# Kernel optimization log

Measured on AMD Instinct MI355X. Metric: run time of the kernel, lower is better.

## Reference

```python
import jax, jax.numpy as jnp
import numpy as np

N = 100000
E = 1600000
NFEAT = 128
NHID1 = 128
NHID2 = 128
NCLASS = 40


def setup_inputs() -> dict:
    key = jax.random.key(0)
    ks = jax.random.split(key, 16)
    x = jax.random.normal(ks[0], (N, NFEAT), dtype=jnp.float32)
    src = jax.random.randint(ks[1], (E,), 0, N, dtype=jnp.int32)
    dst = jax.random.randint(ks[2], (E,), 0, N, dtype=jnp.int32)
    s = 0.05
    params = {
        # SAGE layer 1: self branch and neighbor branch
        'w1s': jax.random.normal(ks[3], (NFEAT, NHID1), dtype=jnp.float32) * s,
        'b1s': jnp.zeros((NHID1,), dtype=jnp.float32),
        'w1n': jax.random.normal(ks[4], (NFEAT, NHID1), dtype=jnp.float32) * s,
        'b1n': jnp.zeros((NHID1,), dtype=jnp.float32),
        # SAGE layer 2 (input dim 2*NHID1)
        'w2s': jax.random.normal(ks[5], (2 * NHID1, NHID2), dtype=jnp.float32) * s,
        'b2s': jnp.zeros((NHID2,), dtype=jnp.float32),
        'w2n': jax.random.normal(ks[6], (2 * NHID1, NHID2), dtype=jnp.float32) * s,
        'b2n': jnp.zeros((NHID2,), dtype=jnp.float32),
        # final linear head (input dim 2*NHID2)
        'wfc': jax.random.normal(ks[7], (2 * NHID2, NCLASS), dtype=jnp.float32) * s,
        'bfc': jnp.zeros((NCLASS,), dtype=jnp.float32),
    }
    return {'x': x, 'src': src, 'dst': dst, **params}


def _neigh_mean(h, src, dst, n_nodes):
    # mean aggregation == spmm(row-normalized adj, h), via segment sum over edges
    msg = jax.ops.segment_sum(h[src], dst, num_segments=n_nodes)  # [N, d]
    cnt = jax.ops.segment_sum(jnp.ones((src.shape[0],), h.dtype), dst, num_segments=n_nodes)
    return msg / jnp.maximum(cnt, 1.0)[:, None]


def _sage_layer(h, src, dst, ws, bs, wn, bn):
    neigh = _neigh_mean(h, src, dst, h.shape[0])
    return jnp.concatenate([h @ ws + bs, neigh @ wn + bn], axis=1)


def _l2_normalize(h, eps=1e-12):
    nrm = jnp.sqrt(jnp.sum(h * h, axis=1, keepdims=True))
    return h / jnp.maximum(nrm, eps)


def reference(x, src, dst, w1s, b1s, w1n, b1n, w2s, b2s, w2n, b2n, wfc, bfc):
    h = jax.nn.relu(_sage_layer(x, src, dst, w1s, b1s, w1n, b1n))  # [N, 2*NHID1]
    h = _l2_normalize(h)
    # dropout is identity in eval mode
    h = jax.nn.relu(_sage_layer(h, src, dst, w2s, b2s, w2n, b2n))  # [N, 2*NHID2]
    h = _l2_normalize(h)
    return h @ wfc + bfc  # [N, NCLASS]
```

## Files before the change

### kernel.cpp

```cpp
#include <hip/hip_runtime.h>
#include <hip/hip_bf16.h>


#define N_NODES 100000
#define N_EDGES 1600000
#define NBUCK   196
#define BCAP    12288
#define CHUNK   4096

typedef unsigned short u16;
typedef unsigned int u32;
typedef __bf16 bf16x8 __attribute__((ext_vector_type(8)));
typedef float  f32x4  __attribute__((ext_vector_type(4)));

__device__ __forceinline__ u16 f2b(float f) {
  unsigned x = __builtin_bit_cast(unsigned, f);
  unsigned r = x + 0x7fffu + ((x >> 16) & 1u);
  return (u16)(r >> 16);
}
__device__ __forceinline__ float b2f(u16 u) {
  return __builtin_bit_cast(float, (unsigned)u << 16);
}
__device__ __forceinline__ bf16x8 ldfrag(const u16* p) {
  uint4 u = *reinterpret_cast<const uint4*>(p);
  return __builtin_bit_cast(bf16x8, u);
}
__device__ __forceinline__ void unpack8(uint4 u, float* f) {
  f[0] = __builtin_bit_cast(float, u.x << 16);
  f[1] = __builtin_bit_cast(float, u.x & 0xffff0000u);
  f[2] = __builtin_bit_cast(float, u.y << 16);
  f[3] = __builtin_bit_cast(float, u.y & 0xffff0000u);
  f[4] = __builtin_bit_cast(float, u.z << 16);
  f[5] = __builtin_bit_cast(float, u.z & 0xffff0000u);
  f[6] = __builtin_bit_cast(float, u.w << 16);
  f[7] = __builtin_bit_cast(float, u.w & 0xffff0000u);
}
__device__ __forceinline__ uint4 pack8(const float* f) {
  uint4 u;
  u.x = (u32)f2b(f[0]) | ((u32)f2b(f[1]) << 16);
  u.y = (u32)f2b(f[2]) | ((u32)f2b(f[3]) << 16);
  u.z = (u32)f2b(f[4]) | ((u32)f2b(f[5]) << 16);
  u.w = (u32)f2b(f[6]) | ((u32)f2b(f[7]) << 16);
  return u;
}

__global__ __launch_bounds__(256) void prep_weights(
    const float* __restrict__ w1s, const float* __restrict__ w1n,
    const float* __restrict__ w2s, const float* __restrict__ w2n,
    const float* __restrict__ wfc,
    u16* __restrict__ WT1, u16* __restrict__ WT2, u16* __restrict__ WFCT) {
  int i = blockIdx.x * 256 + threadIdx.x;
  if (i < 32768) {
    int c = i >> 7, k = i & 127;
    float v = (c < 128) ? w1s[k * 128 + c] : w1n[k * 128 + (c - 128)];
    WT1[c * 128 + k] = f2b(v);
  } else if (i < 32768 + 65536) {
    int j = i - 32768;
    int c = j >> 8, k = j & 255;
    float v = (c < 128) ? w2s[k * 128 + c] : w2n[k * 128 + (c - 128)];
    WT2[c * 256 + k] = f2b(v);
  } else {
    int j = i - 98304;
    int c = j >> 8, k = j & 255;
    float v = (c < 40) ? wfc[k * 40 + c] : 0.f;
    WFCT[c * 256 + k] = f2b(v);
  }
}

__device__ __forceinline__ int wave_incl_scan(int x, int lane) {
#pragma unroll
  for (int d = 1; d < 64; d <<= 1) {
    int n = __shfl_up(x, d, 64);
    if (lane >= d) x += n;
  }
  return x;
}

__global__ __launch_bounds__(256) void bucket_kernel(
    const int* __restrict__ src, const int* __restrict__ dst,
    int* __restrict__ cntg, u32* __restrict__ pairBuf) {
  __shared__ unsigned hist[NBUCK];
  __shared__ unsigned gbase[NBUCK];
  __shared__ int sws[4];
  __shared__ u32 stage[CHUNK];
  __shared__ int tgt[CHUNK];
  const int tid = threadIdx.x, lane = tid & 63, wid = tid >> 6;
  const int e0 = blockIdx.x * CHUNK;

  for (int i = tid; i < NBUCK; i += 256) hist[i] = 0u;
  __syncthreads();

  u32 myW[16];
  int myR[16], myB[16];
#pragma unroll
  for (int k = 0; k < 16; ++k) {
    int e = e0 + k * 256 + tid;
    if (e < N_EDGES) {
      unsigned d = (unsigned)dst[e];
      myW[k] = ((d & 511u) << 17) | (unsigned)src[e];
      myB[k] = (int)(d >> 9);
      myR[k] = (int)atomicAdd(&hist[myB[k]], 1u);
    } else {
      myB[k] = -1;
    }
  }
  __syncthreads();

  int cnt = (tid < NBUCK) ? (int)hist[tid] : 0;
  int inc = wave_incl_scan(cnt, lane);
  if (lane == 63) sws[wid] = inc;
  __syncthreads();
  if (wid == 0) {
    int s = (lane < 4) ? sws[lane] : 0;
    s = wave_incl_scan(s, lane);
    if (lane < 4) sws[lane] = s;
  }
  __syncthreads();
  int excl = (wid ? sws[wid - 1] : 0) + inc - cnt;
  int gofs = 0;
  if (tid < NBUCK && cnt > 0) gofs = tid * BCAP + atomicAdd(&cntg[tid], cnt);
  __syncthreads();
  if (tid < NBUCK) {
    hist[tid] = (unsigned)excl;
    gbase[tid] = (unsigned)gofs;
  }
  __syncthreads();

#pragma unroll
  for (int k = 0; k < 16; ++k) {
    if (myB[k] >= 0) {
      int slot = (int)hist[myB[k]] + myR[k];
      stage[slot] = myW[k];
      tgt[slot] = (int)gbase[myB[k]] + myR[k];
    }
  }
  __syncthreads();
  int nvalid = N_EDGES - e0;
  if (nvalid > CHUNK) nvalid = CHUNK;
  for (int i = tid; i < nvalid; i += 256) pairBuf[tgt[i]] = stage[i];
}

__global__ __launch_bounds__(512) void csr_build(
    const u32* __restrict__ pairBuf, const int* __restrict__ cntg,
    int* __restrict__ rowptr, int* __restrict__ csr) {
  __shared__ int lcnt[512];
  __shared__ int lofs[512];
  __shared__ int sws[8];
  __shared__ int s_eb;
  __shared__ int cstage[10240];
  const int b = blockIdx.x, tid = threadIdx.x;
  const int lane = tid & 63, wid = tid >> 6;

  {
    int v = (tid < b) ? cntg[tid] : 0;
#pragma unroll
    for (int off = 1; off < 64; off <<= 1) v += __shfl_xor(v, off, 64);
    if (lane == 0) sws[wid] = v;
    __syncthreads();
    if (tid == 0) {
      int t = 0;
#pragma unroll
      for (int i = 0; i < 8; ++i) t += sws[i];
      s_eb = t;
    }
    __syncthreads();
  }
  const int eb = s_eb;
  int nb = cntg[b];
  if (nb > BCAP) nb = BCAP;
  if (nb > 10240) nb = 10240;
  const u32* pp = pairBuf + (size_t)b * BCAP;
  __syncthreads();

  lcnt[tid] = 0;
  __syncthreads();
  for (int i = tid; i < nb; i += 512) atomicAdd(&lcnt[(pp[i] >> 17) & 511], 1);
  __syncthreads();
  int v = lcnt[tid];
  int inc = wave_incl_scan(v, lane);
  if (lane == 63) sws[wid] = inc;
  __syncthreads();
  if (wid == 0) {
    int s = (lane < 8) ? sws[lane] : 0;
    s = wave_incl_scan(s, lane);
    if (lane < 8) sws[lane] = s;
  }
  __syncthreads();
  int excl = (wid ? sws[wid - 1] : 0) + inc - v;
  int node = b * 512 + tid;
  if (node <= N_NODES) rowptr[node] = eb + excl;
  lofs[tid] = excl;
  __syncthreads();
  for (int i = tid; i < nb; i += 512) {
    u32 pr = pp[i];
    int pos = atomicAdd(&lofs[(pr >> 17) & 511], 1);
    cstage[pos] = (int)(pr & 0x1FFFFu);
  }
  __syncthreads();
  for (int i = tid; i < nb; i += 512) csr[eb + i] = cstage[i];
}

template <int K, bool AF32>
__global__ __launch_bounds__(256) void gemm_kernel(
    const void* __restrict__ Av, const u16* __restrict__ WT,
    u16* __restrict__ Cs, u16* __restrict__ Cn) {
  constexpr int RB = K * 2;
  constexpr int LOG2RB = (K == 128) ? 8 : 9;
  constexpr int KS = K / 32;
  __shared__ u16 lb[128 * K];

  const int tid = threadIdx.x;
  const int half = blockIdx.x & 1;
  u16* __restrict__ Cout = half ? Cn : Cs;

  const u16* Wsrc = WT + (size_t)half * 128 * K;
  char* lbc = reinterpret_cast<char*>(lb);
#pragma unroll
  for (int i = tid; i < 128 * K / 8; i += 256) {
    uint4 v = *reinterpret_cast<const uint4*>(Wsrc + i * 8);
    int byte = i * 16;
    int swz = byte ^ (((byte >> LOG2RB) & 7) << 4);
    *reinterpret_cast<uint4*>(lbc + swz) = v;
  }
  __syncthreads();

  const int w = tid >> 6, lane = tid & 63;
  const int lrow = lane & 15, lk = lane >> 4;
  const int xr = (lrow & 7) << 4;
  const int stride = gridDim.x >> 1;

  for (int chunk = blockIdx.x >> 1; chunk * 128 < N_NODES; chunk += stride) {
    const int rbase = chunk * 128 + w * 32;
    bf16x8 af[2][KS];
#pragma unroll
    for (int rt = 0; rt < 2; ++rt) {
      int r = rbase + rt * 16 + lrow;
      if (r >= N_NODES) r = N_NODES - 1;
      if constexpr (AF32) {
        const float* ap = (const float*)Av + (size_t)r * K + lk * 8;
#pragma unroll
        for (int ks = 0; ks < KS; ++ks) {
          float4 f0 = *reinterpret_cast<const float4*>(ap + ks * 32);
          float4 f1 = *reinterpret_cast<const float4*>(ap + ks * 32 + 4);
          float f[8] = {f0.x, f0.y, f0.z, f0.w, f1.x, f1.y, f1.z, f1.w};
          af[rt][ks] = __builtin_bit_cast(bf16x8, pack8(f));
        }
      } else {
        const u16* ap = (const u16*)Av + (size_t)r * K + lk * 8;
#pragma unroll
        for (int ks = 0; ks < KS; ++ks) af[rt][ks] = ldfrag(ap + ks * 32);
      }
    }
    f32x4 acc[2][8];
#pragma unroll
    for (int rt = 0; rt < 2; ++rt)
#pragma unroll
      for (int ct = 0; ct < 8; ++ct) acc[rt][ct] = f32x4{0.f, 0.f, 0.f, 0.f};

#pragma unroll
    for (int ks = 0; ks < KS; ++ks) {
#pragma unroll
      for (int ct = 0; ct < 8; ++ct) {
        int byte = (ct * 16 + lrow) * RB + ks * 64 + lk * 16;
        bf16x8 b = __builtin_bit_cast(
            bf16x8, *reinterpret_cast<const uint4*>(lbc + (byte ^ xr)));
        acc[0][ct] = __builtin_amdgcn_mfma_f32_16x16x32_bf16(af[0][ks], b, acc[0][ct], 0, 0, 0);
        acc[1][ct] = __builtin_amdgcn_mfma_f32_16x16x32_bf16(af[1][ks], b, acc[1][ct], 0, 0, 0);
      }
    }
#pragma unroll
    for (int rt = 0; rt < 2; ++rt) {
#pragma unroll
      for (int j = 0; j < 4; ++j) {
        int r = rbase + rt * 16 + lk * 4 + j;
        if (r < N_NODES) {
          u16* cp = Cout + (size_t)r * 128 + lrow;
#pragma unroll
          for (int ct = 0; ct < 8; ++ct) cp[ct * 16] = f2b(acc[rt][ct][j]);
        }
      }
    }
  }
}

__global__ __launch_bounds__(256) void agg_epi_kernel(
    const u16* __restrict__ Xs, const u16* __restrict__ Xn,
    const int* __restrict__ rowptr, const int* __restrict__ csr,
    const float* __restrict__ bs, const float* __restrict__ bn,
    u16* __restrict__ H) {
  int node = (int)((blockIdx.x * 256 + threadIdx.x) >> 6);
  int lane = threadIdx.x & 63;
  if (node >= N_NODES) return;
  const int g = lane >> 4;
  const int lc = lane & 15;
  int beg = rowptr[node], end = rowptr[node + 1];

  float acc[8] = {0.f, 0.f, 0.f, 0.f, 0.f, 0.f, 0.f, 0.f};
  const u16* colbase = Xn + lc * 8;
  for (int j = beg; j < end; j += 4) {
    int e = j + g;
    int s = (e < end) ? csr[e] : 0;
    uint4 u = *reinterpret_cast<const uint4*>(colbase + (size_t)s * 128);
    if (e < end) {
      float f[8];
      unpack8(u, f);
#pragma unroll
      for (int i = 0; i < 8; ++i) acc[i] += f[i];
    }
  }
#pragma unroll
  for (int i = 0; i < 8; ++i) {
    acc[i] += __shfl_xor(acc[i], 32, 64);
    acc[i] += __shfl_xor(acc[i], 16, 64);
  }
  int d = end - beg;
  float inv = 1.f / (float)(d > 0 ? d : 1);

  uint4 sv4 = *reinterpret_cast<const uint4*>(Xs + (size_t)node * 128 + lc * 8);
  float sf[8];
  unpack8(sv4, sf);
  float4 b0 = *reinterpret_cast<const float4*>(bs + lc * 8);
  float4 b1 = *reinterpret_cast<const float4*>(bs + lc * 8 + 4);
  float4 c0 = *reinterpret_cast<const float4*>(bn + lc * 8);
  float4 c1 = *reinterpret_cast<const float4*>(bn + lc * 8 + 4);
  float bsv[8] = {b0.x, b0.y, b0.z, b0.w, b1.x, b1.y, b1.z, b1.w};
  float bnv[8] = {c0.x, c0.y, c0.z, c0.w, c1.x, c1.y, c1.z, c1.w};
  float nf[8];
  float ss = 0.f;
#pragma unroll
  for (int i = 0; i < 8; ++i) {
    sf[i] = fmaxf(sf[i] + bsv[i], 0.f);
    nf[i] = fmaxf(acc[i] * inv + bnv[i], 0.f);
    ss += sf[i] * sf[i] + nf[i] * nf[i];
  }
  ss += __shfl_xor(ss, 1, 64);
  ss += __shfl_xor(ss, 2, 64);
  ss += __shfl_xor(ss, 4, 64);
  ss += __shfl_xor(ss, 8, 64);
  float sc = 1.f / fmaxf(sqrtf(ss), 1e-12f);
#pragma unroll
  for (int i = 0; i < 8; ++i) {
    sf[i] *= sc;
    nf[i] *= sc;
  }
  if (g == 0) {
    *reinterpret_cast<uint4*>(H + (size_t)node * 256 + lc * 8) = pack8(sf);
  } else if (g == 1) {
    *reinterpret_cast<uint4*>(H + (size_t)node * 256 + 128 + lc * 8) = pack8(nf);
  }
}

__global__ __launch_bounds__(256) void fc_kernel(const u16* __restrict__ H2,
                                                 const u16* __restrict__ WFCT,
                                                 const float* __restrict__ bfc,
                                                 float* __restrict__ Out) {
  __shared__ u16 lb[48 * 256];
  char* lbc = reinterpret_cast<char*>(lb);
  const int tid = threadIdx.x;
#pragma unroll
  for (int i = tid; i < 48 * 256 / 8; i += 256) {
    uint4 v = *reinterpret_cast<const uint4*>(WFCT + i * 8);
    int byte = i * 16;
    int swz = byte ^ (((byte >> 9) & 7) << 4);
    *reinterpret_cast<uint4*>(lbc + swz) = v;
  }
  __syncthreads();
  const int w = tid >> 6, lane = tid & 63;
  const int lrow = lane & 15, lk = lane >> 4;
  const int xr = (lrow & 7) << 4;
  const int rbase = blockIdx.x * 64 + w * 16;

  bf16x8 af[8];
  {
    int r = rbase + lrow;
    if (r >= N_NODES) r = N_NODES - 1;
    const u16* ap = H2 + (size_t)r * 256 + lk * 8;
#pragma unroll
    for (int ks = 0; ks < 8; ++ks) af[ks] = ldfrag(ap + ks * 32);
  }
  f32x4 acc[3];
#pragma unroll
  for (int ct = 0; ct < 3; ++ct) acc[ct] = f32x4{0.f, 0.f, 0.f, 0.f};
#pragma unroll
  for (int ks = 0; ks < 8; ++ks) {
#pragma unroll
    for (int ct = 0; ct < 3; ++ct) {
      int byte = (ct * 16 + lrow) * 512 + ks * 64 + lk * 16;
      bf16x8 b = __builtin_bit_cast(
          bf16x8, *reinterpret_cast<const uint4*>(lbc + (byte ^ xr)));
      acc[ct] = __builtin_amdgcn_mfma_f32_16x16x32_bf16(af[ks], b, acc[ct], 0, 0, 0);
    }
  }
#pragma unroll
  for (int j = 0; j < 4; ++j) {
    int r = rbase + lk * 4 + j;
    if (r < N_NODES) {
#pragma unroll
      for (int ct = 0; ct < 3; ++ct) {
        int col = ct * 16 + lrow;
        if (col < 40) Out[(size_t)r * 40 + col] = acc[ct][j] + bfc[col];
      }
    }
  }
}

extern "C" void kernel_launch(void* const* d_in, const int* in_sizes, int n_in,
                              void* d_out, int out_size, void* d_ws, size_t ws_size,
                              hipStream_t stream) {
  const float* x = (const float*)d_in[0];
  const int* src = (const int*)d_in[1];
  const int* dst = (const int*)d_in[2];
  const float* w1s = (const float*)d_in[3];
  const float* b1s = (const float*)d_in[4];
  const float* w1n = (const float*)d_in[5];
  const float* b1n = (const float*)d_in[6];
  const float* w2s = (const float*)d_in[7];
  const float* b2s = (const float*)d_in[8];
  const float* w2n = (const float*)d_in[9];
  const float* b2n = (const float*)d_in[10];
  const float* wfc = (const float*)d_in[11];
  const float* bfc = (const float*)d_in[12];
  float* out = (float*)d_out;

  char* p = (char*)d_ws;
  auto alloc = [&](size_t bytes) {
    char* r = p;
    p += (bytes + 255) & ~(size_t)255;
    return r;
  };
  u16* XWs = (u16*)alloc((size_t)N_NODES * 128 * 2);
  u16* XWn = (u16*)alloc((size_t)N_NODES * 128 * 2);
  u16* h1 = (u16*)alloc((size_t)N_NODES * 256 * 2);
  u16* WT1 = (u16*)alloc(32768 * 2);
  u16* WT2 = (u16*)alloc(65536 * 2);
  u16* WFCT = (u16*)alloc(12288 * 2);
  u32* pairBuf = (u32*)alloc((size_t)NBUCK * BCAP * 4);
  int* cntg = (int*)alloc(NBUCK * 4);
  int* rowptr = (int*)alloc((N_NODES + 1) * 4);
  int* csr = (int*)alloc((size_t)N_EDGES * 4);
  u16* h2 = h1;

  hipMemsetAsync(cntg, 0, NBUCK * 4, stream);
  prep_weights<<<432, 256, 0, stream>>>(w1s, w1n, w2s, w2n, wfc, WT1, WT2, WFCT);
  bucket_kernel<<<391, 256, 0, stream>>>(src, dst, cntg, pairBuf);
  csr_build<<<NBUCK, 512, 0, stream>>>(pairBuf, cntg, rowptr, csr);

  gemm_kernel<128, true><<<1024, 256, 0, stream>>>(x, WT1, XWs, XWn);
  agg_epi_kernel<<<25000, 256, 0, stream>>>(XWs, XWn, rowptr, csr, b1s, b1n, h1);
  gemm_kernel<256, false><<<512, 256, 0, stream>>>(h1, WT2, XWs, XWn);
  agg_epi_kernel<<<25000, 256, 0, stream>>>(XWs, XWn, rowptr, csr, b2s, b2n, h2);
  fc_kernel<<<1563, 256, 0, stream>>>(h2, WFCT, bfc, out);
}
```

Before: 386.1 us.

## Pad CSR rows to multiples of eight, fuse layer-2 aggregation with FC head

Builds a per-bucket padded CSR. Each node's neighbor list is rounded up to a multiple of eight and filled with a dummy node whose XWn row is zeroed, so the aggregation loop runs branch-free and issues two gathers per iteration. The global prefix sum in csr_build and the separate memset are removed. The GEMMs become dedicated 512-thread kernels that compute both halves per block, and the final aggregation is fused with the FC matmul through shared memory so h2 is never written out. The cost is extra padded edge reads and larger CSR storage.

Result: faster. 359.9 us (-6.8%).

```diff
diff --git a/kernel.cpp b/kernel.cpp
--- a/kernel.cpp
+++ b/kernel.cpp
@@ -6,6 +6,7 @@
 #define N_EDGES 1600000
 #define NBUCK   196
 #define BCAP    12288
+#define PB_CAP  14336
 #define CHUNK   4096
 
 typedef unsigned short u16;
@@ -17,9 +18,6 @@
   unsigned x = __builtin_bit_cast(unsigned, f);
   unsigned r = x + 0x7fffu + ((x >> 16) & 1u);
   return (u16)(r >> 16);
-}
-__device__ __forceinline__ float b2f(u16 u) {
-  return __builtin_bit_cast(float, (unsigned)u << 16);
 }
 __device__ __forceinline__ bf16x8 ldfrag(const u16* p) {
   uint4 u = *reinterpret_cast<const uint4*>(p);
@@ -48,7 +46,8 @@
     const float* __restrict__ w1s, const float* __restrict__ w1n,
     const float* __restrict__ w2s, const float* __restrict__ w2n,
     const float* __restrict__ wfc,
-    u16* __restrict__ WT1, u16* __restrict__ WT2, u16* __restrict__ WFCT) {
+    u16* __restrict__ WT1, u16* __restrict__ WT2, u16* __restrict__ WFCT,
+    int* __restrict__ cntg, u16* __restrict__ XWn) {
   int i = blockIdx.x * 256 + threadIdx.x;
   if (i < 32768) {
     int c = i >> 7, k = i & 127;
@@ -59,11 +58,15 @@
     int c = j >> 8, k = j & 255;
     float v = (c < 128) ? w2s[k * 128 + c] : w2n[k * 128 + (c - 128)];
     WT2[c * 256 + k] = f2b(v);
-  } else {
+  } else if (i < 98304 + 12288) {
     int j = i - 98304;
     int c = j >> 8, k = j & 255;
     float v = (c < 40) ? wfc[k * 40 + c] : 0.f;
     WFCT[c * 256 + k] = f2b(v);
+  } else {
+    int t = threadIdx.x;
+    if (t < NBUCK) cntg[t] = 0;
+    if (t >= 128 && t < 256) XWn[(size_t)N_NODES * 128 + (t - 128)] = 0;
   }
 }
 
@@ -142,42 +145,24 @@
 
 __global__ __launch_bounds__(512) void csr_build(
     const u32* __restrict__ pairBuf, const int* __restrict__ cntg,
-    int* __restrict__ rowptr, int* __restrict__ csr) {
+    int* __restrict__ rowptr, int* __restrict__ degA, int* __restrict__ csr) {
   __shared__ int lcnt[512];
   __shared__ int lofs[512];
   __shared__ int sws[8];
-  __shared__ int s_eb;
-  __shared__ int cstage[10240];
+  __shared__ int cstage[PB_CAP];
   const int b = blockIdx.x, tid = threadIdx.x;
   const int lane = tid & 63, wid = tid >> 6;
-
-  {
-    int v = (tid < b) ? cntg[tid] : 0;
-#pragma unroll
-    for (int off = 1; off < 64; off <<= 1) v += __shfl_xor(v, off, 64);
-    if (lane == 0) sws[wid] = v;
-    __syncthreads();
-    if (tid == 0) {
-      int t = 0;
-#pragma unroll
-      for (int i = 0; i < 8; ++i) t += sws[i];
-      s_eb = t;
-    }
-    __syncthreads();
-  }
-  const int eb = s_eb;
   int nb = cntg[b];
   if (nb > BCAP) nb = BCAP;
-  if (nb > 10240) nb = 10240;
   const u32* pp = pairBuf + (size_t)b * BCAP;
-  __syncthreads();
 
   lcnt[tid] = 0;
   __syncthreads();
   for (int i = tid; i < nb; i += 512) atomicAdd(&lcnt[(pp[i] >> 17) & 511], 1);
   __syncthreads();
-  int v = lcnt[tid];
-  int inc = wave_incl_scan(v, lane);
+  int dg = lcnt[tid];
+  int pd = (dg + 7) & ~7;
+  int inc = wave_incl_scan(pd, lane);
   if (lane == 63) sws[wid] = inc;
   __syncthreads();
   if (wid == 0) {
@@ -186,138 +171,57 @@
     if (lane < 8) sws[lane] = s;
   }
   __syncthreads();
-  int excl = (wid ? sws[wid - 1] : 0) + inc - v;
+  int excl = (wid ? sws[wid - 1] : 0) + inc - pd;
+  int ptot = sws[7];
   int node = b * 512 + tid;
-  if (node <= N_NODES) rowptr[node] = eb + excl;
+  if (node < N_NODES) {
+    rowptr[node] = b * PB_CAP + excl;
+    degA[node] = dg;
+  }
   lofs[tid] = excl;
   __syncthreads();
   for (int i = tid; i < nb; i += 512) {
     u32 pr = pp[i];
     int pos = atomicAdd(&lofs[(pr >> 17) & 511], 1);
-    cstage[pos] = (int)(pr & 0x1FFFFu);
-  }
-  __syncthreads();
-  for (int i = tid; i < nb; i += 512) csr[eb + i] = cstage[i];
-}
-
-template <int K, bool AF32>
-__global__ __launch_bounds__(256) void gemm_kernel(
-    const void* __restrict__ Av, const u16* __restrict__ WT,
-    u16* __restrict__ Cs, u16* __restrict__ Cn) {
-  constexpr int RB = K * 2;
-  constexpr int LOG2RB = (K == 128) ? 8 : 9;
-  constexpr int KS = K / 32;
-  __shared__ u16 lb[128 * K];
-
-  const int tid = threadIdx.x;
-  const int half = blockIdx.x & 1;
-  u16* __restrict__ Cout = half ? Cn : Cs;
-
-  const u16* Wsrc = WT + (size_t)half * 128 * K;
-  char* lbc = reinterpret_cast<char*>(lb);
-#pragma unroll
-  for (int i = tid; i < 128 * K / 8; i += 256) {
-    uint4 v = *reinterpret_cast<const uint4*>(Wsrc + i * 8);
-    int byte = i * 16;
-    int swz = byte ^ (((byte >> LOG2RB) & 7) << 4);
-    *reinterpret_cast<uint4*>(lbc + swz) = v;
-  }
-  __syncthreads();
-
-  const int w = tid >> 6, lane = tid & 63;
-  const int lrow = lane & 15, lk = lane >> 4;
-  const int xr = (lrow & 7) << 4;
-  const int stride = gridDim.x >> 1;
-
-  for (int chunk = blockIdx.x >> 1; chunk * 128 < N_NODES; chunk += stride) {
-    const int rbase = chunk * 128 + w * 32;
-    bf16x8 af[2][KS];
-#pragma unroll
-    for (int rt = 0; rt < 2; ++rt) {
-      int r = rbase + rt * 16 + lrow;
-      if (r >= N_NODES) r = N_NODES - 1;
-      if constexpr (AF32) {
-        const float* ap = (const float*)Av + (size_t)r * K + lk * 8;
-#pragma unroll
-        for (int ks = 0; ks < KS; ++ks) {
-          float4 f0 = *reinterpret_cast<const float4*>(ap + ks * 32);
-          float4 f1 = *reinterpret_cast<const float4*>(ap + ks * 32 + 4);
-          float f[8] = {f0.x, f0.y, f0.z, f0.w, f1.x, f1.y, f1.z, f1.w};
-          af[rt][ks] = __builtin_bit_cast(bf16x8, pack8(f));
-        }
-      } else {
-        const u16* ap = (const u16*)Av + (size_t)r * K + lk * 8;
-#pragma unroll
-        for (int ks = 0; ks < KS; ++ks) af[rt][ks] = ldfrag(ap + ks * 32);
-      }
-    }
-    f32x4 acc[2][8];
-#pragma unroll
-    for (int rt = 0; rt < 2; ++rt)
-#pragma unroll
-      for (int ct = 0; ct < 8; ++ct) acc[rt][ct] = f32x4{0.f, 0.f, 0.f, 0.f};
-
-#pragma unroll
-    for (int ks = 0; ks < KS; ++ks) {
-#pragma unroll
-      for (int ct = 0; ct < 8; ++ct) {
-        int byte = (ct * 16 + lrow) * RB + ks * 64 + lk * 16;
-        bf16x8 b = __builtin_bit_cast(
-            bf16x8, *reinterpret_cast<const uint4*>(lbc + (byte ^ xr)));
-        acc[0][ct] = __builtin_amdgcn_mfma_f32_16x16x32_bf16(af[0][ks], b, acc[0][ct], 0, 0, 0);
-        acc[1][ct] = __builtin_amdgcn_mfma_f32_16x16x32_bf16(af[1][ks], b, acc[1][ct], 0, 0, 0);
-      }
-    }
-#pragma unroll
-    for (int rt = 0; rt < 2; ++rt) {
-#pragma unroll
-      for (int j = 0; j < 4; ++j) {
-        int r = rbase + rt * 16 + lk * 4 + j;
-        if (r < N_NODES) {
-          u16* cp = Cout + (size_t)r * 128 + lrow;
-#pragma unroll
-          for (int ct = 0; ct < 8; ++ct) cp[ct * 16] = f2b(acc[rt][ct][j]);
-        }
-      }
-    }
-  }
-}
-
-__global__ __launch_bounds__(256) void agg_epi_kernel(
+    if (pos < PB_CAP) cstage[pos] = (int)(pr & 0x1FFFFu);
+  }
+  __syncthreads();
+  for (int k = excl + dg; k < excl + pd; ++k)
+    if (k < PB_CAP) cstage[k] = N_NODES;
+  __syncthreads();
+  if (ptot > PB_CAP) ptot = PB_CAP;
+  for (int i = tid; i < ptot; i += 512) csr[b * PB_CAP + i] = cstage[i];
+}
+
+__device__ __forceinline__ void agg_node(
     const u16* __restrict__ Xs, const u16* __restrict__ Xn,
-    const int* __restrict__ rowptr, const int* __restrict__ csr,
-    const float* __restrict__ bs, const float* __restrict__ bn,
-    u16* __restrict__ H) {
-  int node = (int)((blockIdx.x * 256 + threadIdx.x) >> 6);
-  int lane = threadIdx.x & 63;
-  if (node >= N_NODES) return;
-  const int g = lane >> 4;
-  const int lc = lane & 15;
-  int beg = rowptr[node], end = rowptr[node + 1];
-
+    const int* __restrict__ rowptr, const int* __restrict__ degA,
+    const int* __restrict__ csr, const float* __restrict__ bs,
+    const float* __restrict__ bn, int node, int g, int lc,
+    float* sf, float* nf) {
+  int beg = rowptr[node], dg = degA[node];
+  int cnt = (dg + 7) & ~7;
   float acc[8] = {0.f, 0.f, 0.f, 0.f, 0.f, 0.f, 0.f, 0.f};
   const u16* colbase = Xn + lc * 8;
-  for (int j = beg; j < end; j += 4) {
-    int e = j + g;
-    int s = (e < end) ? csr[e] : 0;
-    uint4 u = *reinterpret_cast<const uint4*>(colbase + (size_t)s * 128);
-    if (e < end) {
-      float f[8];
-      unpack8(u, f);
-#pragma unroll
-      for (int i = 0; i < 8; ++i) acc[i] += f[i];
-    }
+  const int* cp = csr + beg;
+  for (int j = 0; j < cnt; j += 8) {
+    int s0 = cp[j + g];
+    int s1 = cp[j + 4 + g];
+    uint4 u0 = *reinterpret_cast<const uint4*>(colbase + (size_t)s0 * 128);
+    uint4 u1 = *reinterpret_cast<const uint4*>(colbase + (size_t)s1 * 128);
+    float f0[8], f1[8];
+    unpack8(u0, f0);
+    unpack8(u1, f1);
+#pragma unroll
+    for (int i = 0; i < 8; ++i) acc[i] += f0[i] + f1[i];
   }
 #pragma unroll
   for (int i = 0; i < 8; ++i) {
     acc[i] += __shfl_xor(acc[i], 32, 64);
     acc[i] += __shfl_xor(acc[i], 16, 64);
   }
-  int d = end - beg;
-  float inv = 1.f / (float)(d > 0 ? d : 1);
-
+  float inv = 1.f / (float)(dg > 0 ? dg : 1);
   uint4 sv4 = *reinterpret_cast<const uint4*>(Xs + (size_t)node * 128 + lc * 8);
-  float sf[8];
   unpack8(sv4, sf);
   float4 b0 = *reinterpret_cast<const float4*>(bs + lc * 8);
   float4 b1 = *reinterpret_cast<const float4*>(bs + lc * 8 + 4);
@@ -325,7 +229,6 @@
   float4 c1 = *reinterpret_cast<const float4*>(bn + lc * 8 + 4);
   float bsv[8] = {b0.x, b0.y, b0.z, b0.w, b1.x, b1.y, b1.z, b1.w};
   float bnv[8] = {c0.x, c0.y, c0.z, c0.w, c1.x, c1.y, c1.z, c1.w};
-  float nf[8];
   float ss = 0.f;
 #pragma unroll
   for (int i = 0; i < 8; ++i) {
@@ -343,6 +246,19 @@
     sf[i] *= sc;
     nf[i] *= sc;
   }
+}
+
+__global__ __launch_bounds__(256) void agg_epi_kernel(
+    const u16* __restrict__ Xs, const u16* __restrict__ Xn,
+    const int* __restrict__ rowptr, const int* __restrict__ degA,
+    const int* __restrict__ csr, const float* __restrict__ bs,
+    const float* __restrict__ bn, u16* __restrict__ H) {
+  int node = (int)((blockIdx.x * 256 + threadIdx.x) >> 6);
+  int lane = threadIdx.x & 63;
+  if (node >= N_NODES) return;
+  const int g = lane >> 4, lc = lane & 15;
+  float sf[8], nf[8];
+  agg_node(Xs, Xn, rowptr, degA, csr, bs, bn, node, g, lc, sf, nf);
   if (g == 0) {
     *reinterpret_cast<uint4*>(H + (size_t)node * 256 + lc * 8) = pack8(sf);
   } else if (g == 1) {
@@ -350,57 +266,177 @@
   }
 }
 
-__global__ __launch_bounds__(256) void fc_kernel(const u16* __restrict__ H2,
-                                                 const u16* __restrict__ WFCT,
-                                                 const float* __restrict__ bfc,
-                                                 float* __restrict__ Out) {
-  __shared__ u16 lb[48 * 256];
+__global__ __launch_bounds__(512) void agg_fc_kernel(
+    const u16* __restrict__ Xs, const u16* __restrict__ Xn,
+    const int* __restrict__ rowptr, const int* __restrict__ degA,
+    const int* __restrict__ csr, const float* __restrict__ bs,
+    const float* __restrict__ bn, const u16* __restrict__ WFCT,
+    const float* __restrict__ bfc, float* __restrict__ Out) {
+  __shared__ u16 hh[32][264];
+  __shared__ u16 wf[48][264];
+  const int tid = threadIdx.x, w = tid >> 6, lane = tid & 63;
+  const int g = lane >> 4, lc = lane & 15;
+  const int nb0 = blockIdx.x * 32;
+
+  for (int i = tid; i < 1536; i += 512) {
+    int row = i >> 5, col = (i & 31) * 8;
+    *reinterpret_cast<uint4*>(&wf[row][col]) =
+        *reinterpret_cast<const uint4*>(WFCT + row * 256 + col);
+  }
+
+  for (int t = 0; t < 4; ++t) {
+    int r = w * 4 + t;
+    int node = nb0 + r;
+    if (node < N_NODES) {
+      float sf[8], nf[8];
+      agg_node(Xs, Xn, rowptr, degA, csr, bs, bn, node, g, lc, sf, nf);
+      if (g == 0) {
+        *reinterpret_cast<uint4*>(&hh[r][lc * 8]) = pack8(sf);
+      } else if (g == 1) {
+        *reinterpret_cast<uint4*>(&hh[r][128 + lc * 8]) = pack8(nf);
+      }
+    } else {
+      uint4 z = {0u, 0u, 0u, 0u};
+      if (g == 0) *reinterpret_cast<uint4*>(&hh[r][lc * 8]) = z;
+      else if (g == 1) *reinterpret_cast<uint4*>(&hh[r][128 + lc * 8]) = z;
+    }
+  }
+  __syncthreads();
+
+  const int rt = w & 1, cg = w >> 1;
+  if (cg < 3) {
+    const int lrow = lane & 15, lk = lane >> 4;
+    f32x4 acc = {0.f, 0.f, 0.f, 0.f};
+#pragma unroll
+    for (int ks = 0; ks < 8; ++ks) {
+      bf16x8 a = ldfrag(&hh[rt * 16 + lrow][ks * 32 + lk * 8]);
+      bf16x8 b = ldfrag(&wf[cg * 16 + lrow][ks * 32 + lk * 8]);
+      acc = __builtin_amdgcn_mfma_f32_16x16x32_bf16(a, b, acc, 0, 0, 0);
+    }
+#pragma unroll
+    for (int j = 0; j < 4; ++j) {
+      int row = nb0 + rt * 16 + lk * 4 + j;
+      int col = cg * 16 + lrow;
+      if (row < N_NODES && col < 40) Out[(size_t)row * 40 + col] = acc[j] + bfc[col];
+    }
+  }
+}
+
+__global__ __launch_bounds__(512) void gemm1_kernel(
+    const float* __restrict__ A, const u16* __restrict__ WT,
+    u16* __restrict__ Cs, u16* __restrict__ Cn) {
+  __shared__ u16 lb[256 * 128];
   char* lbc = reinterpret_cast<char*>(lb);
   const int tid = threadIdx.x;
-#pragma unroll
-  for (int i = tid; i < 48 * 256 / 8; i += 256) {
-    uint4 v = *reinterpret_cast<const uint4*>(WFCT + i * 8);
+  for (int i = tid; i < 4096; i += 512) {
+    uint4 v = *reinterpret_cast<const uint4*>(WT + i * 8);
     int byte = i * 16;
-    int swz = byte ^ (((byte >> 9) & 7) << 4);
+    int swz = byte ^ (((byte >> 8) & 7) << 4);
     *reinterpret_cast<uint4*>(lbc + swz) = v;
   }
-  __syncthreads();
+
   const int w = tid >> 6, lane = tid & 63;
   const int lrow = lane & 15, lk = lane >> 4;
   const int xr = (lrow & 7) << 4;
-  const int rbase = blockIdx.x * 64 + w * 16;
+  const int rbase = blockIdx.x * 128 + w * 16;
+
+  bf16x8 af[4];
+  {
+    int r = rbase + lrow;
+    if (r >= N_NODES) r = N_NODES - 1;
+    const float* ap = A + (size_t)r * 128 + lk * 8;
+#pragma unroll
+    for (int ks = 0; ks < 4; ++ks) {
+      float4 f0 = *reinterpret_cast<const float4*>(ap + ks * 32);
+      float4 f1 = *reinterpret_cast<const float4*>(ap + ks * 32 + 4);
+      float f[8] = {f0.x, f0.y, f0.z, f0.w, f1.x, f1.y, f1.z, f1.w};
+      af[ks] = __builtin_bit_cast(bf16x8, pack8(f));
+    }
+  }
+  __syncthreads();
+
+  f32x4 acc[16];
+#pragma unroll
+  for (int ct = 0; ct < 16; ++ct) acc[ct] = f32x4{0.f, 0.f, 0.f, 0.f};
+#pragma unroll
+  for (int ks = 0; ks < 4; ++ks) {
+#pragma unroll
+    for (int ct = 0; ct < 16; ++ct) {
+      int byte = (ct * 16 + lrow) * 256 + ks * 64 + lk * 16;
+      bf16x8 b = __builtin_bit_cast(
+          bf16x8, *reinterpret_cast<const uint4*>(lbc + (byte ^ xr)));
+      acc[ct] = __builtin_amdgcn_mfma_f32_16x16x32_bf16(af[ks], b, acc[ct], 0, 0, 0);
+    }
+  }
+#pragma unroll
+  for (int j = 0; j < 4; ++j) {
+    int r = rbase + lk * 4 + j;
+    if (r < N_NODES) {
+      u16* cs = Cs + (size_t)r * 128 + lrow;
+      u16* cn = Cn + (size_t)r * 128 + lrow;
+#pragma unroll
+      for (int ct = 0; ct < 8; ++ct) cs[ct * 16] = f2b(acc[ct][j]);
+#pragma unroll
+      for (int ct = 0; ct < 8; ++ct) cn[ct * 16] = f2b(acc[8 + ct][j]);
+    }
+  }
+}
+
+__global__ __launch_bounds__(512) void gemm2_kernel(
+    const u16* __restrict__ A, const u16* __restrict__ WT,
+    u16* __restrict__ Cs, u16* __restrict__ Cn) {
+  __shared__ u16 lb[128 * 256];
+  char* lbc = reinterpret_cast<char*>(lb);
+  const int tid = threadIdx.x;
+  const int w = tid >> 6, lane = tid & 63;
+  const int lrow = lane & 15, lk = lane >> 4;
+  const int xr = (lrow & 7) << 4;
+  const int rbase = blockIdx.x * 128 + w * 16;
 
   bf16x8 af[8];
   {
     int r = rbase + lrow;
     if (r >= N_NODES) r = N_NODES - 1;
-    const u16* ap = H2 + (size_t)r * 256 + lk * 8;
+    const u16* ap = A + (size_t)r * 256 + lk * 8;
 #pragma unroll
     for (int ks = 0; ks < 8; ++ks) af[ks] = ldfrag(ap + ks * 32);
   }
-  f32x4 acc[3];
-#pragma unroll
-  for (int ct = 0; ct < 3; ++ct) acc[ct] = f32x4{0.f, 0.f, 0.f, 0.f};
-#pragma unroll
-  for (int ks = 0; ks < 8; ++ks) {
-#pragma unroll
-    for (int ct = 0; ct < 3; ++ct) {
-      int byte = (ct * 16 + lrow) * 512 + ks * 64 + lk * 16;
-      bf16x8 b = __builtin_bit_cast(
-          bf16x8, *reinterpret_cast<const uint4*>(lbc + (byte ^ xr)));
-      acc[ct] = __builtin_amdgcn_mfma_f32_16x16x32_bf16(af[ks], b, acc[ct], 0, 0, 0);
-    }
-  }
-#pragma unroll
-  for (int j = 0; j < 4; ++j) {
-    int r = rbase + lk * 4 + j;
-    if (r < N_NODES) {
-#pragma unroll
-      for (int ct = 0; ct < 3; ++ct) {
-        int col = ct * 16 + lrow;
-        if (col < 40) Out[(size_t)r * 40 + col] = acc[ct][j] + bfc[col];
+
+#pragma unroll
+  for (int half = 0; half < 2; ++half) {
+    const u16* Wsrc = WT + (size_t)half * 128 * 256;
+    for (int i = tid; i < 4096; i += 512) {
+      uint4 v = *reinterpret_cast<const uint4*>(Wsrc + i * 8);
+      int byte = i * 16;
+      int swz = byte ^ (((byte >> 9) & 7) << 4);
+      *reinterpret_cast<uint4*>(lbc + swz) = v;
+    }
+    __syncthreads();
+
+    f32x4 acc[8];
+#pragma unroll
+    for (int ct = 0; ct < 8; ++ct) acc[ct] = f32x4{0.f, 0.f, 0.f, 0.f};
+#pragma unroll
+    for (int ks = 0; ks < 8; ++ks) {
+#pragma unroll
+      for (int ct = 0; ct < 8; ++ct) {
+        int byte = (ct * 16 + lrow) * 512 + ks * 64 + lk * 16;
+        bf16x8 b = __builtin_bit_cast(
+            bf16x8, *reinterpret_cast<const uint4*>(lbc + (byte ^ xr)));
+        acc[ct] = __builtin_amdgcn_mfma_f32_16x16x32_bf16(af[ks], b, acc[ct], 0, 0, 0);
       }
     }
+    u16* __restrict__ Cout = half ? Cn : Cs;
+#pragma unroll
+    for (int j = 0; j < 4; ++j) {
+      int r = rbase + lk * 4 + j;
+      if (r < N_NODES) {
+        u16* cp = Cout + (size_t)r * 128 + lrow;
+#pragma unroll
+        for (int ct = 0; ct < 8; ++ct) cp[ct * 16] = f2b(acc[ct][j]);
+      }
+    }
+    __syncthreads();
   }
 }
 
@@ -429,25 +465,25 @@
     return r;
   };
   u16* XWs = (u16*)alloc((size_t)N_NODES * 128 * 2);
-  u16* XWn = (u16*)alloc((size_t)N_NODES * 128 * 2);
+  u16* XWn = (u16*)alloc(((size_t)N_NODES + 1) * 128 * 2);
   u16* h1 = (u16*)alloc((size_t)N_NODES * 256 * 2);
   u16* WT1 = (u16*)alloc(32768 * 2);
   u16* WT2 = (u16*)alloc(65536 * 2);
   u16* WFCT = (u16*)alloc(12288 * 2);
   u32* pairBuf = (u32*)alloc((size_t)NBUCK * BCAP * 4);
   int* cntg = (int*)alloc(NBUCK * 4);
-  int* rowptr = (int*)alloc((N_NODES + 1) * 4);
-  int* csr = (int*)alloc((size_t)N_EDGES * 4);
-  u16* h2 = h1;
-
-  hipMemsetAsync(cntg, 0, NBUCK * 4, stream);
-  prep_weights<<<432, 256, 0, stream>>>(w1s, w1n, w2s, w2n, wfc, WT1, WT2, WFCT);
+  int* rowptr = (int*)alloc((size_t)N_NODES * 4);
+  int* degA = (int*)alloc((size_t)N_NODES * 4);
+  int* csr = (int*)alloc((size_t)NBUCK * PB_CAP * 4);
+
+  prep_weights<<<433, 256, 0, stream>>>(w1s, w1n, w2s, w2n, wfc, WT1, WT2, WFCT,
+                                        cntg, XWn);
   bucket_kernel<<<391, 256, 0, stream>>>(src, dst, cntg, pairBuf);
-  csr_build<<<NBUCK, 512, 0, stream>>>(pairBuf, cntg, rowptr, csr);
-
-  gemm_kernel<128, true><<<1024, 256, 0, stream>>>(x, WT1, XWs, XWn);
-  agg_epi_kernel<<<25000, 256, 0, stream>>>(XWs, XWn, rowptr, csr, b1s, b1n, h1);
-  gemm_kernel<256, false><<<512, 256, 0, stream>>>(h1, WT2, XWs, XWn);
-  agg_epi_kernel<<<25000, 256, 0, stream>>>(XWs, XWn, rowptr, csr, b2s, b2n, h2);
-  fc_kernel<<<1563, 256, 0, stream>>>(h2, WFCT, bfc, out);
-}
+  csr_build<<<NBUCK, 512, 0, stream>>>(pairBuf, cntg, rowptr, degA, csr);
+
+  gemm1_kernel<<<782, 512, 0, stream>>>(x, WT1, XWs, XWn);
+  agg_epi_kernel<<<25000, 256, 0, stream>>>(XWs, XWn, rowptr, degA, csr, b1s, b1n, h1);
+  gemm2_kernel<<<782, 512, 0, stream>>>(h1, WT2, XWs, XWn);
+  agg_fc_kernel<<<3125, 512, 0, stream>>>(XWs, XWn, rowptr, degA, csr, b2s, b2n,
+                                          WFCT, bfc, out);
+}
```
